# Optimization experiments

Measured on AMD Instinct MI355X. Metric: run time of the kernel, lower is better.

Reference implementation:

```python
import jax, jax.numpy as jnp
import numpy as np

B, K, D = 8192, 50, 64
NU, NV = 100000, 100000


def setup_inputs() -> dict:
    key = jax.random.key(0)
    ks = jax.random.split(key, 9)
    nodes = jax.random.randint(ks[0], (B,), 0, NU)
    history = jax.random.randint(ks[1], (B, K), 0, NV)
    degrees = jax.random.randint(ks[2], (B,), 1, K + 1)  # 1..K actual neighbors per node
    u_to_e = jax.random.normal(ks[3], (NU, D), dtype=jnp.float32)
    v_to_e = jax.random.normal(ks[4], (NV, D), dtype=jnp.float32)
    s1 = 1.0 / np.sqrt(2 * D)
    s2 = 1.0 / np.sqrt(D)
    att1_w = jax.random.normal(ks[5], (D, 2 * D), dtype=jnp.float32) * s1
    att2_w = jax.random.normal(ks[6], (D, D), dtype=jnp.float32) * s2
    att3_w = jax.random.normal(ks[7], (1, D), dtype=jnp.float32) * s2
    return {
        "nodes": nodes, "history": history, "degrees": degrees,
        "u_to_e": u_to_e, "v_to_e": v_to_e,
        "att1_w": att1_w, "att1_b": jnp.zeros((D,), jnp.float32),
        "att2_w": att2_w, "att2_b": jnp.zeros((D,), jnp.float32),
        "att3_w": att3_w, "att3_b": jnp.zeros((1,), jnp.float32),
    }


def reference(nodes, history, degrees, u_to_e, v_to_e,
              att1_w, att1_b, att2_w, att2_b, att3_w, att3_b):
    # uv=True: neighbors are items (v_to_e), self representation from u_to_e.
    neigh = v_to_e[history]                      # [B, K, D] gathered neighbor embeddings
    self_e = u_to_e[nodes]                       # [B, D]
    self_rep = jnp.broadcast_to(self_e[:, None, :], neigh.shape)
    x = jnp.concatenate([neigh, self_rep], axis=-1)        # [B, K, 2D]
    h = jax.nn.relu(jnp.einsum('bkf,df->bkd', x, att1_w) + att1_b)
    h = jax.nn.relu(jnp.einsum('bkd,ed->bke', h, att2_w) + att2_b)
    logits = (jnp.einsum('bkd,od->bko', h, att3_w) + att3_b)[..., 0]  # [B, K]
    # Softmax over the true (ragged) neighbor set only.
    mask = jnp.arange(K)[None, :] < degrees[:, None]       # [B, K] bool
    logits = jnp.where(mask, logits, -1e9)
    att = jax.nn.softmax(logits, axis=1) * mask            # [B, K]
    return jnp.einsum('bkd,bk->bd', neigh, att)            # [B, D]
```

## Files before the change

### kernel.cpp

```cpp
#include <hip/hip_runtime.h>
#include <cstdint>
#include <cstddef>

constexpr int D = 64;
constexpr int TWO_D = 128;

typedef __attribute__((ext_vector_type(8))) short bf16x8;
typedef __attribute__((ext_vector_type(4))) float f32x4;
typedef __attribute__((ext_vector_type(4))) unsigned short u16x4;

static __device__ __forceinline__ short f2bf(float x) {
    unsigned u = __builtin_bit_cast(unsigned, x);
    u += 0x7fffu + ((u >> 16) & 1u);
    return (short)(u >> 16);
}
static __device__ __forceinline__ float bf2f(unsigned short h) {
    return __builtin_bit_cast(float, ((unsigned)h) << 16);
}
static __device__ __forceinline__ bf16x8 cvt8(const float* p) {
    const float4 a = *(const float4*)p;
    const float4 c = *(const float4*)(p + 4);
    bf16x8 f;
    f[0] = f2bf(a.x); f[1] = f2bf(a.y); f[2] = f2bf(a.z); f[3] = f2bf(a.w);
    f[4] = f2bf(c.x); f[5] = f2bf(c.y); f[6] = f2bf(c.z); f[7] = f2bf(c.w);
    return f;
}

__global__ __launch_bounds__(256) void proj_s(
    const float* __restrict__ u_to_e, const int* __restrict__ nodes,
    const float* __restrict__ att1_w, const float* __restrict__ att1_b,
    const float* __restrict__ att2_w,
    float* __restrict__ S, unsigned short* __restrict__ W1F,
    unsigned short* __restrict__ W2F,
    int Bn, int nSB)
{
    const int tid = threadIdx.x;

    if ((int)blockIdx.x == nSB) {
        if (tid < 64) {
            const int plg = tid >> 4, plc = tid & 15;
#pragma unroll
            for (int tc = 0; tc < 4; ++tc)
#pragma unroll
                for (int ks = 0; ks < 2; ++ks) {
                    const bf16x8 f1 = cvt8(
                        att1_w + (tc * 16 + plc) * TWO_D + ks * 32 + plg * 8);
                    *(bf16x8*)(W1F + ((size_t)(tc * 2 + ks) * 64 + tid) * 8) = f1;
                    const bf16x8 f2 = cvt8(
                        att2_w + (tc * 16 + plc) * D + ks * 32 + plg * 8);
                    *(bf16x8*)(W2F + ((size_t)(tc * 2 + ks) * 64 + tid) * 8) = f2;
                }
        }
        return;
    }

    constexpr int ST = 68;
    __shared__ float xs[64 * ST];
    __shared__ float ws[64 * ST];

    const int base = (int)blockIdx.x * 64;

#pragma unroll
    for (int it = 0; it < 4; ++it) {
        const int flat = it * 256 + tid;
        const int dd = flat >> 4, f4 = flat & 15;
        const float4 w = *(const float4*)(att1_w + dd * TWO_D + D + f4 * 4);
        ws[(f4 * 4 + 0) * ST + dd] = w.x;
        ws[(f4 * 4 + 1) * ST + dd] = w.y;
        ws[(f4 * 4 + 2) * ST + dd] = w.z;
        ws[(f4 * 4 + 3) * ST + dd] = w.w;
    }
#pragma unroll
    for (int it = 0; it < 4; ++it) {
        const int flat = it * 256 + tid;
        const int r = flat >> 4, f4 = flat & 15;
        int gr = base + r;
        if (gr >= Bn) gr = Bn - 1;
        const int row = nodes[gr];
        const float4 x = *(const float4*)(u_to_e + (size_t)row * D + f4 * 4);
        xs[(f4 * 4 + 0) * ST + r] = x.x;
        xs[(f4 * 4 + 1) * ST + r] = x.y;
        xs[(f4 * 4 + 2) * ST + r] = x.z;
        xs[(f4 * 4 + 3) * ST + r] = x.w;
    }
    __syncthreads();

    const int d0 = (tid & 15) * 4;
    const int r0 = (tid >> 4) * 4;
    float acc[4][4];
#pragma unroll
    for (int i = 0; i < 4; ++i)
#pragma unroll
        for (int j = 0; j < 4; ++j) acc[i][j] = 0.f;

#pragma unroll 8
    for (int f = 0; f < D; ++f) {
        const float4 w = *(const float4*)&ws[f * ST + d0];
        const float4 x = *(const float4*)&xs[f * ST + r0];
        const float wv[4] = {w.x, w.y, w.z, w.w};
        const float xv[4] = {x.x, x.y, x.z, x.w};
#pragma unroll
        for (int ri = 0; ri < 4; ++ri)
#pragma unroll
            for (int di = 0; di < 4; ++di)
                acc[ri][di] += xv[ri] * wv[di];
    }

    float bv[4];
#pragma unroll
    for (int di = 0; di < 4; ++di) bv[di] = att1_b[d0 + di];
#pragma unroll
    for (int ri = 0; ri < 4; ++ri) {
        const int gr = base + r0 + ri;
        if (gr < Bn) {
            float4 o = {acc[ri][0] + bv[0], acc[ri][1] + bv[1],
                        acc[ri][2] + bv[2], acc[ri][3] + bv[3]};
            *(float4*)(S + (size_t)gr * D + d0) = o;
        }
    }
}

__global__ __launch_bounds__(256) void agg_fused(
    const int* __restrict__ history, const int* __restrict__ degrees,
    const float* __restrict__ v_to_e,
    const float* __restrict__ att2_b, const float* __restrict__ att3_w,
    const float* __restrict__ S,
    const unsigned short* __restrict__ W1F,
    const unsigned short* __restrict__ W2F,
    float* __restrict__ out, int Bn, int K)
{
    __shared__ unsigned short hldsb[4][16 * 72];
    __shared__ float red[4][64];
    __shared__ float mxs[4];
    __shared__ float sms[4];

    const int b     = (int)blockIdx.x;
    const int wslot = threadIdx.x >> 6;
    const int l     = threadIdx.x & 63;
    const int lg    = l >> 4;
    const int lc    = l & 15;
    const int deg   = degrees[b];
    const bool live = (wslot * 16 < deg);
    const bool act  = (wslot * 16 + lc < deg);

    int kk = wslot * 16 + lc;
    if (kk > K - 1) kk = K - 1;
    const int vrow = history[(size_t)b * K + kk];

    float4 vr4[4];
    if (live) {
#pragma unroll
        for (int jj = 0; jj < 4; ++jj) {
            const int row = __shfl(vrow, jj * 4 + lg);
            vr4[jj] = *(const float4*)(v_to_e + (size_t)row * D + lc * 4);
        }
    }

    float m_w = -1e30f, ex = 0.f;
    float4 acc4 = {0.f, 0.f, 0.f, 0.f};
    if (live) {
        const float* vp = v_to_e + (size_t)vrow * D;
        const bf16x8 bv0 = cvt8(vp + lg * 8);
        const bf16x8 bv1 = cvt8(vp + 32 + lg * 8);

        unsigned short* hrow = &hldsb[wslot][0];
#pragma unroll
        for (int tc = 0; tc < 4; ++tc) {
            f32x4 hacc = (f32x4)0.f;
            const bf16x8 w10 = *(const bf16x8*)(
                W1F + ((size_t)(tc * 2 + 0) * 64 + l) * 8);
            hacc = __builtin_amdgcn_mfma_f32_16x16x32_bf16(w10, bv0, hacc, 0, 0, 0);
            const bf16x8 w11 = *(const bf16x8*)(
                W1F + ((size_t)(tc * 2 + 1) * 64 + l) * 8);
            hacc = __builtin_amdgcn_mfma_f32_16x16x32_bf16(w11, bv1, hacc, 0, 0, 0);
            const float4 sv = *(const float4*)(S + (size_t)b * D + tc * 16 + lg * 4);
            u16x4 hb;
            hb[0] = (unsigned short)f2bf(fmaxf(hacc[0] + sv.x, 0.f));
            hb[1] = (unsigned short)f2bf(fmaxf(hacc[1] + sv.y, 0.f));
            hb[2] = (unsigned short)f2bf(fmaxf(hacc[2] + sv.z, 0.f));
            hb[3] = (unsigned short)f2bf(fmaxf(hacc[3] + sv.w, 0.f));
            *(u16x4*)&hrow[lc * 72 + tc * 16 + lg * 4] = hb;
        }

        const bf16x8 af0 = *(const bf16x8*)&hrow[lc * 72 + lg * 8];
        const bf16x8 af1 = *(const bf16x8*)&hrow[lc * 72 + 32 + lg * 8];

        float part = 0.f;
#pragma unroll
        for (int tc = 0; tc < 4; ++tc) {
            f32x4 acc = (f32x4)0.f;
            const bf16x8 w0 = *(const bf16x8*)(
                W2F + ((size_t)(tc * 2 + 0) * 64 + l) * 8);
            acc = __builtin_amdgcn_mfma_f32_16x16x32_bf16(w0, af0, acc, 0, 0, 0);
            const bf16x8 w1 = *(const bf16x8*)(
                W2F + ((size_t)(tc * 2 + 1) * 64 + l) * 8);
            acc = __builtin_amdgcn_mfma_f32_16x16x32_bf16(w1, af1, acc, 0, 0, 0);
            const float4 b2v = *(const float4*)(att2_b + tc * 16 + lg * 4);
            const float4 w3v = *(const float4*)(att3_w + tc * 16 + lg * 4);
            part += fmaxf(acc[0] + b2v.x, 0.f) * w3v.x;
            part += fmaxf(acc[1] + b2v.y, 0.f) * w3v.y;
            part += fmaxf(acc[2] + b2v.z, 0.f) * w3v.z;
            part += fmaxf(acc[3] + b2v.w, 0.f) * w3v.w;
        }
        part += __shfl_xor(part, 16);
        part += __shfl_xor(part, 32);
        const float logit = act ? part : -1e30f;

        m_w = logit;
#pragma unroll
        for (int off = 1; off < 16; off <<= 1)
            m_w = fmaxf(m_w, __shfl_xor(m_w, off));
        ex = act ? __expf(logit - m_w) : 0.f;
        float s_w = ex;
#pragma unroll
        for (int off = 1; off < 16; off <<= 1)
            s_w += __shfl_xor(s_w, off);
        if (l == 0) { mxs[wslot] = m_w; sms[wslot] = s_w; }

#pragma unroll
        for (int jj = 0; jj < 4; ++jj) {
            const float a = __shfl(ex, jj * 4 + lg);
            acc4.x += a * vr4[jj].x;
            acc4.y += a * vr4[jj].y;
            acc4.z += a * vr4[jj].z;
            acc4.w += a * vr4[jj].w;
        }
        acc4.x += __shfl_xor(acc4.x, 16); acc4.x += __shfl_xor(acc4.x, 32);
        acc4.y += __shfl_xor(acc4.y, 16); acc4.y += __shfl_xor(acc4.y, 32);
        acc4.z += __shfl_xor(acc4.z, 16); acc4.z += __shfl_xor(acc4.z, 32);
        acc4.w += __shfl_xor(acc4.w, 16); acc4.w += __shfl_xor(acc4.w, 32);
    } else {
        if (l == 0) { mxs[wslot] = -1e30f; sms[wslot] = 0.f; }
    }

    __syncthreads();
    const float m = fmaxf(fmaxf(mxs[0], mxs[1]), fmaxf(mxs[2], mxs[3]));
    const float tot = sms[0] * __expf(mxs[0] - m) + sms[1] * __expf(mxs[1] - m)
                    + sms[2] * __expf(mxs[2] - m) + sms[3] * __expf(mxs[3] - m);
    const float scale = live ? __expf(m_w - m) / tot : 0.f;

    const float comp = (lg == 0) ? acc4.x : (lg == 1) ? acc4.y
                     : (lg == 2) ? acc4.z : acc4.w;
    red[wslot][lc * 4 + lg] = comp * scale;
    __syncthreads();
    if (wslot == 0)
        out[(size_t)b * D + l] =
            (red[0][l] + red[1][l]) + (red[2][l] + red[3][l]);
}

__global__ __launch_bounds__(256) void agg_fallback(
    const int* __restrict__ nodes, const int* __restrict__ history,
    const int* __restrict__ degrees,
    const float* __restrict__ u_to_e, const float* __restrict__ v_to_e,
    const float* __restrict__ att1_w, const float* __restrict__ att1_b,
    const float* __restrict__ att2_w, const float* __restrict__ att2_b,
    const float* __restrict__ att3_w, const float* __restrict__ att3_b,
    float* __restrict__ out, int Bn, int K)
{
    const int b    = (int)((blockIdx.x * blockDim.x + threadIdx.x) >> 6);
    const int lane = threadIdx.x & 63;
    if (b >= Bn) return;

    const int  deg    = degrees[b];
    const bool active = (lane < deg);
    const int  v      = history[(size_t)b * K + ((lane < K) ? lane : 0)];

    float h1[D];
    float vr[D];
    const float4* v4 = (const float4*)(v_to_e + (size_t)v * D);
#pragma unroll
    for (int i = 0; i < D / 4; ++i) {
        float4 t = v4[i];
        vr[4 * i + 0] = t.x; vr[4 * i + 1] = t.y;
        vr[4 * i + 2] = t.z; vr[4 * i + 3] = t.w;
    }
    const float* urow = u_to_e + (size_t)nodes[b] * D;
#pragma unroll
    for (int d = 0; d < D; ++d) {
        const float* w1 = att1_w + d * TWO_D;
        float a0 = att1_b[d], a1 = 0.f, a2 = 0.f, a3 = 0.f;
#pragma unroll
        for (int f = 0; f < D; f += 4) {
            a0 += vr[f + 0] * w1[f + 0];
            a1 += vr[f + 1] * w1[f + 1];
            a2 += vr[f + 2] * w1[f + 2];
            a3 += vr[f + 3] * w1[f + 3];
            a0 += urow[f + 0] * w1[D + f + 0];
            a1 += urow[f + 1] * w1[D + f + 1];
            a2 += urow[f + 2] * w1[D + f + 2];
            a3 += urow[f + 3] * w1[D + f + 3];
        }
        h1[d] = fmaxf((a0 + a1) + (a2 + a3), 0.f);
    }

    float logit = att3_b[0];
#pragma unroll 4
    for (int e = 0; e < D; ++e) {
        const float* w2r = att2_w + e * D;
        float a0 = 0.f, a1 = 0.f, a2 = 0.f, a3 = 0.f;
#pragma unroll
        for (int dd = 0; dd < D; dd += 4) {
            a0 += h1[dd + 0] * w2r[dd + 0];
            a1 += h1[dd + 1] * w2r[dd + 1];
            a2 += h1[dd + 2] * w2r[dd + 2];
            a3 += h1[dd + 3] * w2r[dd + 3];
        }
        float h2 = (a0 + a1) + (a2 + a3) + att2_b[e];
        logit += fmaxf(h2, 0.f) * att3_w[e];
    }

    float ml = active ? logit : -1e30f;
#pragma unroll
    for (int off = 32; off > 0; off >>= 1) ml = fmaxf(ml, __shfl_xor(ml, off));
    const float ex = active ? __expf(logit - ml) : 0.f;
    float smv = ex;
#pragma unroll
    for (int off = 32; off > 0; off >>= 1) smv += __shfl_xor(smv, off);
    const float att = ex / smv;

    float acc = 0.f;
    for (int kk = 0; kk < deg; ++kk) {
        const float a  = __shfl(att, kk);
        const int   vk = __shfl(v, kk);
        acc += a * v_to_e[(size_t)vk * D + lane];
    }
    out[(size_t)b * D + lane] = acc;
}

extern "C" void kernel_launch(void* const* d_in, const int* in_sizes, int n_in,
                              void* d_out, int out_size, void* d_ws, size_t ws_size,
                              hipStream_t stream)
{
    const int*   nodes   = (const int*)d_in[0];
    const int*   history = (const int*)d_in[1];
    const int*   degrees = (const int*)d_in[2];
    const float* u_to_e  = (const float*)d_in[3];
    const float* v_to_e  = (const float*)d_in[4];
    const float* att1_w  = (const float*)d_in[5];
    const float* att1_b  = (const float*)d_in[6];
    const float* att2_w  = (const float*)d_in[7];
    const float* att2_b  = (const float*)d_in[8];
    const float* att3_w  = (const float*)d_in[9];
    const float* att3_b  = (const float*)d_in[10];
    float*       out     = (float*)d_out;

    const int Bn = in_sizes[0];
    const int K  = in_sizes[1] / Bn;

    const size_t s_bytes   = (size_t)Bn * D * sizeof(float);
    const size_t wf_bytes  = (size_t)8 * 64 * 8 * sizeof(unsigned short);
    const size_t need = s_bytes + 2 * wf_bytes;

    if (ws_size >= need) {
        char* p = (char*)d_ws;
        float*          S   = (float*)p;            p += s_bytes;
        unsigned short* W1F = (unsigned short*)p;   p += wf_bytes;
        unsigned short* W2F = (unsigned short*)p;
        const int nSB = (Bn + 63) / 64;
        proj_s<<<nSB + 1, 256, 0, stream>>>(
            u_to_e, nodes, att1_w, att1_b, att2_w, S, W1F, W2F, Bn, nSB);
        agg_fused<<<Bn, 256, 0, stream>>>(
            history, degrees, v_to_e, att2_b, att3_w,
            S, W1F, W2F, out, Bn, K);
    } else {
        const int agg_blocks = (Bn * 64 + 255) / 256;
        agg_fallback<<<agg_blocks, 256, 0, stream>>>(
            nodes, history, degrees, u_to_e, v_to_e,
            att1_w, att1_b, att2_w, att2_b, att3_w, att3_b,
            out, Bn, K);
    }
}
```

Before: 43.95 us.

## Process four nodes per block and prefetch next node's neighbor embeddings

Each block of agg_fused now handles four consecutive batch rows instead of one. Inside the loop it issues the gathers of the next row's history and neighbor embeddings, into registers, in the middle of the current row's two MLP stages. This overlaps gather latency with MFMA work and cuts block launch overhead. In exchange the grid shrinks to a quarter of the blocks, which may lower memory-level parallelism across the GPU, and register pressure rises from the doubled prefetch buffers.

```diff
diff --git a/kernel.cpp b/kernel.cpp
--- a/kernel.cpp
+++ b/kernel.cpp
@@ -4,6 +4,7 @@
 
 constexpr int D = 64;
 constexpr int TWO_D = 128;
+constexpr int NB = 4;
 
 typedef __attribute__((ext_vector_type(8))) short bf16x8;
 typedef __attribute__((ext_vector_type(4))) float f32x4;
@@ -20,6 +21,12 @@
 static __device__ __forceinline__ bf16x8 cvt8(const float* p) {
     const float4 a = *(const float4*)p;
     const float4 c = *(const float4*)(p + 4);
+    bf16x8 f;
+    f[0] = f2bf(a.x); f[1] = f2bf(a.y); f[2] = f2bf(a.z); f[3] = f2bf(a.w);
+    f[4] = f2bf(c.x); f[5] = f2bf(c.y); f[6] = f2bf(c.z); f[7] = f2bf(c.w);
+    return f;
+}
+static __device__ __forceinline__ bf16x8 pack2(const float4& a, const float4& c) {
     bf16x8 f;
     f[0] = f2bf(a.x); f[1] = f2bf(a.y); f[2] = f2bf(a.z); f[3] = f2bf(a.w);
     f[4] = f2bf(c.x); f[5] = f2bf(c.y); f[6] = f2bf(c.z); f[7] = f2bf(c.w);
@@ -134,118 +141,164 @@
     __shared__ float mxs[4];
     __shared__ float sms[4];
 
-    const int b     = (int)blockIdx.x;
     const int wslot = threadIdx.x >> 6;
     const int l     = threadIdx.x & 63;
     const int lg    = l >> 4;
     const int lc    = l & 15;
-    const int deg   = degrees[b];
-    const bool live = (wslot * 16 < deg);
-    const bool act  = (wslot * 16 + lc < deg);
-
-    int kk = wslot * 16 + lc;
-    if (kk > K - 1) kk = K - 1;
-    const int vrow = history[(size_t)b * K + kk];
-
+
+    int kpos = wslot * 16 + lc;
+    if (kpos > K - 1) kpos = K - 1;
+
+    const int b0 = (int)blockIdx.x * NB;
+
+    int    deg  = 0, vrow = 0;
     float4 vr4[4];
-    if (live) {
-#pragma unroll
-        for (int jj = 0; jj < 4; ++jj) {
-            const int row = __shfl(vrow, jj * 4 + lg);
-            vr4[jj] = *(const float4*)(v_to_e + (size_t)row * D + lc * 4);
-        }
-    }
-
-    float m_w = -1e30f, ex = 0.f;
-    float4 acc4 = {0.f, 0.f, 0.f, 0.f};
-    if (live) {
-        const float* vp = v_to_e + (size_t)vrow * D;
-        const bf16x8 bv0 = cvt8(vp + lg * 8);
-        const bf16x8 bv1 = cvt8(vp + 32 + lg * 8);
-
-        unsigned short* hrow = &hldsb[wslot][0];
-#pragma unroll
-        for (int tc = 0; tc < 4; ++tc) {
-            f32x4 hacc = (f32x4)0.f;
-            const bf16x8 w10 = *(const bf16x8*)(
-                W1F + ((size_t)(tc * 2 + 0) * 64 + l) * 8);
-            hacc = __builtin_amdgcn_mfma_f32_16x16x32_bf16(w10, bv0, hacc, 0, 0, 0);
-            const bf16x8 w11 = *(const bf16x8*)(
-                W1F + ((size_t)(tc * 2 + 1) * 64 + l) * 8);
-            hacc = __builtin_amdgcn_mfma_f32_16x16x32_bf16(w11, bv1, hacc, 0, 0, 0);
-            const float4 sv = *(const float4*)(S + (size_t)b * D + tc * 16 + lg * 4);
-            u16x4 hb;
-            hb[0] = (unsigned short)f2bf(fmaxf(hacc[0] + sv.x, 0.f));
-            hb[1] = (unsigned short)f2bf(fmaxf(hacc[1] + sv.y, 0.f));
-            hb[2] = (unsigned short)f2bf(fmaxf(hacc[2] + sv.z, 0.f));
-            hb[3] = (unsigned short)f2bf(fmaxf(hacc[3] + sv.w, 0.f));
-            *(u16x4*)&hrow[lc * 72 + tc * 16 + lg * 4] = hb;
-        }
-
-        const bf16x8 af0 = *(const bf16x8*)&hrow[lc * 72 + lg * 8];
-        const bf16x8 af1 = *(const bf16x8*)&hrow[lc * 72 + 32 + lg * 8];
-
-        float part = 0.f;
-#pragma unroll
-        for (int tc = 0; tc < 4; ++tc) {
-            f32x4 acc = (f32x4)0.f;
-            const bf16x8 w0 = *(const bf16x8*)(
-                W2F + ((size_t)(tc * 2 + 0) * 64 + l) * 8);
-            acc = __builtin_amdgcn_mfma_f32_16x16x32_bf16(w0, af0, acc, 0, 0, 0);
-            const bf16x8 w1 = *(const bf16x8*)(
-                W2F + ((size_t)(tc * 2 + 1) * 64 + l) * 8);
-            acc = __builtin_amdgcn_mfma_f32_16x16x32_bf16(w1, af1, acc, 0, 0, 0);
-            const float4 b2v = *(const float4*)(att2_b + tc * 16 + lg * 4);
-            const float4 w3v = *(const float4*)(att3_w + tc * 16 + lg * 4);
-            part += fmaxf(acc[0] + b2v.x, 0.f) * w3v.x;
-            part += fmaxf(acc[1] + b2v.y, 0.f) * w3v.y;
-            part += fmaxf(acc[2] + b2v.z, 0.f) * w3v.z;
-            part += fmaxf(acc[3] + b2v.w, 0.f) * w3v.w;
-        }
-        part += __shfl_xor(part, 16);
-        part += __shfl_xor(part, 32);
-        const float logit = act ? part : -1e30f;
-
-        m_w = logit;
-#pragma unroll
-        for (int off = 1; off < 16; off <<= 1)
-            m_w = fmaxf(m_w, __shfl_xor(m_w, off));
-        ex = act ? __expf(logit - m_w) : 0.f;
-        float s_w = ex;
-#pragma unroll
-        for (int off = 1; off < 16; off <<= 1)
-            s_w += __shfl_xor(s_w, off);
-        if (l == 0) { mxs[wslot] = m_w; sms[wslot] = s_w; }
-
-#pragma unroll
-        for (int jj = 0; jj < 4; ++jj) {
-            const float a = __shfl(ex, jj * 4 + lg);
-            acc4.x += a * vr4[jj].x;
-            acc4.y += a * vr4[jj].y;
-            acc4.z += a * vr4[jj].z;
-            acc4.w += a * vr4[jj].w;
-        }
-        acc4.x += __shfl_xor(acc4.x, 16); acc4.x += __shfl_xor(acc4.x, 32);
-        acc4.y += __shfl_xor(acc4.y, 16); acc4.y += __shfl_xor(acc4.y, 32);
-        acc4.z += __shfl_xor(acc4.z, 16); acc4.z += __shfl_xor(acc4.z, 32);
-        acc4.w += __shfl_xor(acc4.w, 16); acc4.w += __shfl_xor(acc4.w, 32);
-    } else {
-        if (l == 0) { mxs[wslot] = -1e30f; sms[wslot] = 0.f; }
-    }
-
-    __syncthreads();
-    const float m = fmaxf(fmaxf(mxs[0], mxs[1]), fmaxf(mxs[2], mxs[3]));
-    const float tot = sms[0] * __expf(mxs[0] - m) + sms[1] * __expf(mxs[1] - m)
-                    + sms[2] * __expf(mxs[2] - m) + sms[3] * __expf(mxs[3] - m);
-    const float scale = live ? __expf(m_w - m) / tot : 0.f;
-
-    const float comp = (lg == 0) ? acc4.x : (lg == 1) ? acc4.y
-                     : (lg == 2) ? acc4.z : acc4.w;
-    red[wslot][lc * 4 + lg] = comp * scale;
-    __syncthreads();
-    if (wslot == 0)
-        out[(size_t)b * D + l] =
-            (red[0][l] + red[1][l]) + (red[2][l] + red[3][l]);
+    float4 bvr[4];
+    if (b0 < Bn) {
+        deg  = degrees[b0];
+        vrow = history[(size_t)b0 * K + kpos];
+        if (wslot * 16 < deg) {
+#pragma unroll
+            for (int jj = 0; jj < 4; ++jj) {
+                const int row = __shfl(vrow, jj * 4 + lg);
+                vr4[jj] = *(const float4*)(v_to_e + (size_t)row * D + lc * 4);
+            }
+            const float* vp = v_to_e + (size_t)vrow * D;
+            bvr[0] = *(const float4*)(vp + lg * 8);
+            bvr[1] = *(const float4*)(vp + lg * 8 + 4);
+            bvr[2] = *(const float4*)(vp + 32 + lg * 8);
+            bvr[3] = *(const float4*)(vp + 32 + lg * 8 + 4);
+        }
+    }
+
+    for (int i = 0; i < NB; ++i) {
+        const int  bcur  = b0 + i;
+        const bool valid = (bcur < Bn);
+        const bool live  = valid && (wslot * 16 < deg);
+        const bool act   = valid && (wslot * 16 + lc < deg);
+
+        const int  bnext  = bcur + 1;
+        const bool validN = (i + 1 < NB) && (bnext < Bn);
+        int degN = 0, vrowN = 0;
+        if (validN) {
+            degN  = degrees[bnext];
+            vrowN = history[(size_t)bnext * K + kpos];
+        }
+
+        float m_w = -1e30f, ex = 0.f;
+        float4 acc4 = {0.f, 0.f, 0.f, 0.f};
+
+        bf16x8 af0, af1;
+        if (live) {
+            const bf16x8 bv0 = pack2(bvr[0], bvr[1]);
+            const bf16x8 bv1 = pack2(bvr[2], bvr[3]);
+            unsigned short* hrow = &hldsb[wslot][0];
+#pragma unroll
+            for (int tc = 0; tc < 4; ++tc) {
+                f32x4 hacc = (f32x4)0.f;
+                const bf16x8 w10 = *(const bf16x8*)(
+                    W1F + ((size_t)(tc * 2 + 0) * 64 + l) * 8);
+                hacc = __builtin_amdgcn_mfma_f32_16x16x32_bf16(w10, bv0, hacc, 0, 0, 0);
+                const bf16x8 w11 = *(const bf16x8*)(
+                    W1F + ((size_t)(tc * 2 + 1) * 64 + l) * 8);
+                hacc = __builtin_amdgcn_mfma_f32_16x16x32_bf16(w11, bv1, hacc, 0, 0, 0);
+                const float4 sv = *(const float4*)(S + (size_t)bcur * D + tc * 16 + lg * 4);
+                u16x4 hb;
+                hb[0] = (unsigned short)f2bf(fmaxf(hacc[0] + sv.x, 0.f));
+                hb[1] = (unsigned short)f2bf(fmaxf(hacc[1] + sv.y, 0.f));
+                hb[2] = (unsigned short)f2bf(fmaxf(hacc[2] + sv.z, 0.f));
+                hb[3] = (unsigned short)f2bf(fmaxf(hacc[3] + sv.w, 0.f));
+                *(u16x4*)&hrow[lc * 72 + tc * 16 + lg * 4] = hb;
+            }
+            af0 = *(const bf16x8*)&hrow[lc * 72 + lg * 8];
+            af1 = *(const bf16x8*)&hrow[lc * 72 + 32 + lg * 8];
+        }
+
+        float4 vr4n[4];
+        float4 bvrn[4];
+        const bool liveN = validN && (wslot * 16 < degN);
+        if (liveN) {
+#pragma unroll
+            for (int jj = 0; jj < 4; ++jj) {
+                const int row = __shfl(vrowN, jj * 4 + lg);
+                vr4n[jj] = *(const float4*)(v_to_e + (size_t)row * D + lc * 4);
+            }
+            const float* vp = v_to_e + (size_t)vrowN * D;
+            bvrn[0] = *(const float4*)(vp + lg * 8);
+            bvrn[1] = *(const float4*)(vp + lg * 8 + 4);
+            bvrn[2] = *(const float4*)(vp + 32 + lg * 8);
+            bvrn[3] = *(const float4*)(vp + 32 + lg * 8 + 4);
+        }
+
+        if (live) {
+            float part = 0.f;
+#pragma unroll
+            for (int tc = 0; tc < 4; ++tc) {
+                f32x4 acc = (f32x4)0.f;
+                const bf16x8 w0 = *(const bf16x8*)(
+                    W2F + ((size_t)(tc * 2 + 0) * 64 + l) * 8);
+                acc = __builtin_amdgcn_mfma_f32_16x16x32_bf16(w0, af0, acc, 0, 0, 0);
+                const bf16x8 w1 = *(const bf16x8*)(
+                    W2F + ((size_t)(tc * 2 + 1) * 64 + l) * 8);
+                acc = __builtin_amdgcn_mfma_f32_16x16x32_bf16(w1, af1, acc, 0, 0, 0);
+                const float4 b2v = *(const float4*)(att2_b + tc * 16 + lg * 4);
+                const float4 w3v = *(const float4*)(att3_w + tc * 16 + lg * 4);
+                part += fmaxf(acc[0] + b2v.x, 0.f) * w3v.x;
+                part += fmaxf(acc[1] + b2v.y, 0.f) * w3v.y;
+                part += fmaxf(acc[2] + b2v.z, 0.f) * w3v.z;
+                part += fmaxf(acc[3] + b2v.w, 0.f) * w3v.w;
+            }
+            part += __shfl_xor(part, 16);
+            part += __shfl_xor(part, 32);
+            const float logit = act ? part : -1e30f;
+
+            m_w = logit;
+#pragma unroll
+            for (int off = 1; off < 16; off <<= 1)
+                m_w = fmaxf(m_w, __shfl_xor(m_w, off));
+            ex = act ? __expf(logit - m_w) : 0.f;
+            float s_w = ex;
+#pragma unroll
+            for (int off = 1; off < 16; off <<= 1)
+                s_w += __shfl_xor(s_w, off);
+            if (l == 0) { mxs[wslot] = m_w; sms[wslot] = s_w; }
+
+#pragma unroll
+            for (int jj = 0; jj < 4; ++jj) {
+                const float a = __shfl(ex, jj * 4 + lg);
+                acc4.x += a * vr4[jj].x;
+                acc4.y += a * vr4[jj].y;
+                acc4.z += a * vr4[jj].z;
+                acc4.w += a * vr4[jj].w;
+            }
+            acc4.x += __shfl_xor(acc4.x, 16); acc4.x += __shfl_xor(acc4.x, 32);
+            acc4.y += __shfl_xor(acc4.y, 16); acc4.y += __shfl_xor(acc4.y, 32);
+            acc4.z += __shfl_xor(acc4.z, 16); acc4.z += __shfl_xor(acc4.z, 32);
+            acc4.w += __shfl_xor(acc4.w, 16); acc4.w += __shfl_xor(acc4.w, 32);
+        } else if (valid) {
+            if (l == 0) { mxs[wslot] = -1e30f; sms[wslot] = 0.f; }
+        }
+
+        if (valid) {
+            __syncthreads();
+            const float m = fmaxf(fmaxf(mxs[0], mxs[1]), fmaxf(mxs[2], mxs[3]));
+            const float tot = sms[0] * __expf(mxs[0] - m) + sms[1] * __expf(mxs[1] - m)
+                            + sms[2] * __expf(mxs[2] - m) + sms[3] * __expf(mxs[3] - m);
+            const float scale = live ? __expf(m_w - m) / tot : 0.f;
+            const float comp = (lg == 0) ? acc4.x : (lg == 1) ? acc4.y
+                             : (lg == 2) ? acc4.z : acc4.w;
+            red[wslot][lc * 4 + lg] = comp * scale;
+            __syncthreads();
+            if (wslot == 0)
+                out[(size_t)bcur * D + l] =
+                    (red[0][l] + red[1][l]) + (red[2][l] + red[3][l]);
+        }
+
+        deg  = degN;
+        vrow = vrowN;
+#pragma unroll
+        for (int jj = 0; jj < 4; ++jj) { vr4[jj] = vr4n[jj]; bvr[jj] = bvrn[jj]; }
+    }
 }
 
 __global__ __launch_bounds__(256) void agg_fallback(
@@ -359,7 +412,7 @@
         const int nSB = (Bn + 63) / 64;
         proj_s<<<nSB + 1, 256, 0, stream>>>(
             u_to_e, nodes, att1_w, att1_b, att2_w, S, W1F, W2F, Bn, nSB);
-        agg_fused<<<Bn, 256, 0, stream>>>(
+        agg_fused<<<(Bn + NB - 1) / NB, 256, 0, stream>>>(
             history, degrees, v_to_e, att2_b, att3_w,
             S, W1F, W2F, out, Bn, K);
     } else {
```

Result: slower. 59.09 us (+34.5%).

## Process one batch row per wave with online softmax and prefetched tiles

Applied to the files above, without the earlier changes.

The aggregation kernel now assigns one batch row to each wave instead of one row per 256-thread block. Each wave loops over up to four 16-neighbor tiles, keeping an online softmax (running max and sum) and prefetching the next tile's embeddings into registers while the current tile is computed. Block-wide shared-memory reductions and both __syncthreads are removed, and waves whose tiles fall past the degree no longer sit idle. The cost is serial per-wave latency across tiles and higher register pressure from the double-buffered float4 arrays.

```diff
diff --git a/kernel.cpp b/kernel.cpp
--- a/kernel.cpp
+++ b/kernel.cpp
@@ -14,12 +14,15 @@
     u += 0x7fffu + ((u >> 16) & 1u);
     return (short)(u >> 16);
 }
-static __device__ __forceinline__ float bf2f(unsigned short h) {
-    return __builtin_bit_cast(float, ((unsigned)h) << 16);
-}
 static __device__ __forceinline__ bf16x8 cvt8(const float* p) {
     const float4 a = *(const float4*)p;
     const float4 c = *(const float4*)(p + 4);
+    bf16x8 f;
+    f[0] = f2bf(a.x); f[1] = f2bf(a.y); f[2] = f2bf(a.z); f[3] = f2bf(a.w);
+    f[4] = f2bf(c.x); f[5] = f2bf(c.y); f[6] = f2bf(c.z); f[7] = f2bf(c.w);
+    return f;
+}
+static __device__ __forceinline__ bf16x8 pack2(const float4& a, const float4& c) {
     bf16x8 f;
     f[0] = f2bf(a.x); f[1] = f2bf(a.y); f[2] = f2bf(a.z); f[3] = f2bf(a.w);
     f[4] = f2bf(c.x); f[5] = f2bf(c.y); f[6] = f2bf(c.z); f[7] = f2bf(c.w);
@@ -120,7 +123,7 @@
     }
 }
 
-__global__ __launch_bounds__(256) void agg_fused(
+__global__ __launch_bounds__(256) void agg_wave(
     const int* __restrict__ history, const int* __restrict__ degrees,
     const float* __restrict__ v_to_e,
     const float* __restrict__ att2_b, const float* __restrict__ att3_w,
@@ -130,122 +133,146 @@
     float* __restrict__ out, int Bn, int K)
 {
     __shared__ unsigned short hldsb[4][16 * 72];
-    __shared__ float red[4][64];
-    __shared__ float mxs[4];
-    __shared__ float sms[4];
-
-    const int b     = (int)blockIdx.x;
+
     const int wslot = threadIdx.x >> 6;
-    const int l     = threadIdx.x & 63;
-    const int lg    = l >> 4;
-    const int lc    = l & 15;
-    const int deg   = degrees[b];
-    const bool live = (wslot * 16 < deg);
-    const bool act  = (wslot * 16 + lc < deg);
-
-    int kk = wslot * 16 + lc;
-    if (kk > K - 1) kk = K - 1;
-    const int vrow = history[(size_t)b * K + kk];
-
-    float4 vr4[4];
-    if (live) {
+    const int b     = (int)blockIdx.x * 4 + wslot;
+    if (b >= Bn) return;
+    const int l  = threadIdx.x & 63;
+    const int lg = l >> 4;
+    const int lc = l & 15;
+    const int deg = degrees[b];
+
+    int vrow[4];
+#pragma unroll
+    for (int t = 0; t < 4; ++t) {
+        int kp = t * 16 + lc;
+        if (kp > K - 1) kp = K - 1;
+        vrow[t] = history[(size_t)b * K + kp];
+    }
+
+    float4 sv[4], b2v[4], w3v[4];
+#pragma unroll
+    for (int tc = 0; tc < 4; ++tc) {
+        sv[tc]  = *(const float4*)(S + (size_t)b * D + tc * 16 + lg * 4);
+        b2v[tc] = *(const float4*)(att2_b + tc * 16 + lg * 4);
+        w3v[tc] = *(const float4*)(att3_w + tc * 16 + lg * 4);
+    }
+
+    unsigned short* hrow = &hldsb[wslot][0];
+
+    float4 bvr[2][4];
+    float4 vr4[2][4];
+
+    {
+        const float* vp = v_to_e + (size_t)vrow[0] * D;
+        bvr[0][0] = *(const float4*)(vp + lg * 8);
+        bvr[0][1] = *(const float4*)(vp + lg * 8 + 4);
+        bvr[0][2] = *(const float4*)(vp + 32 + lg * 8);
+        bvr[0][3] = *(const float4*)(vp + 32 + lg * 8 + 4);
 #pragma unroll
         for (int jj = 0; jj < 4; ++jj) {
-            const int row = __shfl(vrow, jj * 4 + lg);
-            vr4[jj] = *(const float4*)(v_to_e + (size_t)row * D + lc * 4);
-        }
-    }
-
-    float m_w = -1e30f, ex = 0.f;
+            const int row = __shfl(vrow[0], jj * 4 + lg);
+            vr4[0][jj] = *(const float4*)(v_to_e + (size_t)row * D + lc * 4);
+        }
+    }
+
+    float m_run = -1e30f, s_run = 0.f;
     float4 acc4 = {0.f, 0.f, 0.f, 0.f};
-    if (live) {
-        const float* vp = v_to_e + (size_t)vrow * D;
-        const bf16x8 bv0 = cvt8(vp + lg * 8);
-        const bf16x8 bv1 = cvt8(vp + 32 + lg * 8);
-
-        unsigned short* hrow = &hldsb[wslot][0];
-#pragma unroll
-        for (int tc = 0; tc < 4; ++tc) {
-            f32x4 hacc = (f32x4)0.f;
-            const bf16x8 w10 = *(const bf16x8*)(
-                W1F + ((size_t)(tc * 2 + 0) * 64 + l) * 8);
-            hacc = __builtin_amdgcn_mfma_f32_16x16x32_bf16(w10, bv0, hacc, 0, 0, 0);
-            const bf16x8 w11 = *(const bf16x8*)(
-                W1F + ((size_t)(tc * 2 + 1) * 64 + l) * 8);
-            hacc = __builtin_amdgcn_mfma_f32_16x16x32_bf16(w11, bv1, hacc, 0, 0, 0);
-            const float4 sv = *(const float4*)(S + (size_t)b * D + tc * 16 + lg * 4);
-            u16x4 hb;
-            hb[0] = (unsigned short)f2bf(fmaxf(hacc[0] + sv.x, 0.f));
-            hb[1] = (unsigned short)f2bf(fmaxf(hacc[1] + sv.y, 0.f));
-            hb[2] = (unsigned short)f2bf(fmaxf(hacc[2] + sv.z, 0.f));
-            hb[3] = (unsigned short)f2bf(fmaxf(hacc[3] + sv.w, 0.f));
-            *(u16x4*)&hrow[lc * 72 + tc * 16 + lg * 4] = hb;
-        }
-
-        const bf16x8 af0 = *(const bf16x8*)&hrow[lc * 72 + lg * 8];
-        const bf16x8 af1 = *(const bf16x8*)&hrow[lc * 72 + 32 + lg * 8];
-
-        float part = 0.f;
-#pragma unroll
-        for (int tc = 0; tc < 4; ++tc) {
-            f32x4 acc = (f32x4)0.f;
-            const bf16x8 w0 = *(const bf16x8*)(
-                W2F + ((size_t)(tc * 2 + 0) * 64 + l) * 8);
-            acc = __builtin_amdgcn_mfma_f32_16x16x32_bf16(w0, af0, acc, 0, 0, 0);
-            const bf16x8 w1 = *(const bf16x8*)(
-                W2F + ((size_t)(tc * 2 + 1) * 64 + l) * 8);
-            acc = __builtin_amdgcn_mfma_f32_16x16x32_bf16(w1, af1, acc, 0, 0, 0);
-            const float4 b2v = *(const float4*)(att2_b + tc * 16 + lg * 4);
-            const float4 w3v = *(const float4*)(att3_w + tc * 16 + lg * 4);
-            part += fmaxf(acc[0] + b2v.x, 0.f) * w3v.x;
-            part += fmaxf(acc[1] + b2v.y, 0.f) * w3v.y;
-            part += fmaxf(acc[2] + b2v.z, 0.f) * w3v.z;
-            part += fmaxf(acc[3] + b2v.w, 0.f) * w3v.w;
-        }
-        part += __shfl_xor(part, 16);
-        part += __shfl_xor(part, 32);
-        const float logit = act ? part : -1e30f;
-
-        m_w = logit;
-#pragma unroll
-        for (int off = 1; off < 16; off <<= 1)
-            m_w = fmaxf(m_w, __shfl_xor(m_w, off));
-        ex = act ? __expf(logit - m_w) : 0.f;
-        float s_w = ex;
-#pragma unroll
-        for (int off = 1; off < 16; off <<= 1)
-            s_w += __shfl_xor(s_w, off);
-        if (l == 0) { mxs[wslot] = m_w; sms[wslot] = s_w; }
-
-#pragma unroll
-        for (int jj = 0; jj < 4; ++jj) {
-            const float a = __shfl(ex, jj * 4 + lg);
-            acc4.x += a * vr4[jj].x;
-            acc4.y += a * vr4[jj].y;
-            acc4.z += a * vr4[jj].z;
-            acc4.w += a * vr4[jj].w;
-        }
-        acc4.x += __shfl_xor(acc4.x, 16); acc4.x += __shfl_xor(acc4.x, 32);
-        acc4.y += __shfl_xor(acc4.y, 16); acc4.y += __shfl_xor(acc4.y, 32);
-        acc4.z += __shfl_xor(acc4.z, 16); acc4.z += __shfl_xor(acc4.z, 32);
-        acc4.w += __shfl_xor(acc4.w, 16); acc4.w += __shfl_xor(acc4.w, 32);
-    } else {
-        if (l == 0) { mxs[wslot] = -1e30f; sms[wslot] = 0.f; }
-    }
-
-    __syncthreads();
-    const float m = fmaxf(fmaxf(mxs[0], mxs[1]), fmaxf(mxs[2], mxs[3]));
-    const float tot = sms[0] * __expf(mxs[0] - m) + sms[1] * __expf(mxs[1] - m)
-                    + sms[2] * __expf(mxs[2] - m) + sms[3] * __expf(mxs[3] - m);
-    const float scale = live ? __expf(m_w - m) / tot : 0.f;
+
+#pragma unroll
+    for (int t = 0; t < 4; ++t) {
+        if (t * 16 < deg) {
+            const int cur = t & 1, nxt = cur ^ 1;
+
+            if (t + 1 < 4 && (t + 1) * 16 < deg) {
+                const float* vp = v_to_e + (size_t)vrow[t + 1] * D;
+                bvr[nxt][0] = *(const float4*)(vp + lg * 8);
+                bvr[nxt][1] = *(const float4*)(vp + lg * 8 + 4);
+                bvr[nxt][2] = *(const float4*)(vp + 32 + lg * 8);
+                bvr[nxt][3] = *(const float4*)(vp + 32 + lg * 8 + 4);
+#pragma unroll
+                for (int jj = 0; jj < 4; ++jj) {
+                    const int row = __shfl(vrow[t + 1], jj * 4 + lg);
+                    vr4[nxt][jj] = *(const float4*)(v_to_e + (size_t)row * D + lc * 4);
+                }
+            }
+
+            const bf16x8 bv0 = pack2(bvr[cur][0], bvr[cur][1]);
+            const bf16x8 bv1 = pack2(bvr[cur][2], bvr[cur][3]);
+#pragma unroll
+            for (int tc = 0; tc < 4; ++tc) {
+                f32x4 hacc = (f32x4)0.f;
+                const bf16x8 w10 = *(const bf16x8*)(
+                    W1F + ((size_t)(tc * 2 + 0) * 64 + l) * 8);
+                hacc = __builtin_amdgcn_mfma_f32_16x16x32_bf16(w10, bv0, hacc, 0, 0, 0);
+                const bf16x8 w11 = *(const bf16x8*)(
+                    W1F + ((size_t)(tc * 2 + 1) * 64 + l) * 8);
+                hacc = __builtin_amdgcn_mfma_f32_16x16x32_bf16(w11, bv1, hacc, 0, 0, 0);
+                u16x4 hb;
+                hb[0] = (unsigned short)f2bf(fmaxf(hacc[0] + sv[tc].x, 0.f));
+                hb[1] = (unsigned short)f2bf(fmaxf(hacc[1] + sv[tc].y, 0.f));
+                hb[2] = (unsigned short)f2bf(fmaxf(hacc[2] + sv[tc].z, 0.f));
+                hb[3] = (unsigned short)f2bf(fmaxf(hacc[3] + sv[tc].w, 0.f));
+                *(u16x4*)&hrow[lc * 72 + tc * 16 + lg * 4] = hb;
+            }
+            const bf16x8 af0 = *(const bf16x8*)&hrow[lc * 72 + lg * 8];
+            const bf16x8 af1 = *(const bf16x8*)&hrow[lc * 72 + 32 + lg * 8];
+
+            float part = 0.f;
+#pragma unroll
+            for (int tc = 0; tc < 4; ++tc) {
+                f32x4 acc = (f32x4)0.f;
+                const bf16x8 w0 = *(const bf16x8*)(
+                    W2F + ((size_t)(tc * 2 + 0) * 64 + l) * 8);
+                acc = __builtin_amdgcn_mfma_f32_16x16x32_bf16(w0, af0, acc, 0, 0, 0);
+                const bf16x8 w1 = *(const bf16x8*)(
+                    W2F + ((size_t)(tc * 2 + 1) * 64 + l) * 8);
+                acc = __builtin_amdgcn_mfma_f32_16x16x32_bf16(w1, af1, acc, 0, 0, 0);
+                part += fmaxf(acc[0] + b2v[tc].x, 0.f) * w3v[tc].x;
+                part += fmaxf(acc[1] + b2v[tc].y, 0.f) * w3v[tc].y;
+                part += fmaxf(acc[2] + b2v[tc].z, 0.f) * w3v[tc].z;
+                part += fmaxf(acc[3] + b2v[tc].w, 0.f) * w3v[tc].w;
+            }
+            part += __shfl_xor(part, 16);
+            part += __shfl_xor(part, 32);
+            const bool actk = (t * 16 + lc < deg);
+            const float logit = actk ? part : -1e30f;
+
+            float mt = logit;
+#pragma unroll
+            for (int off = 1; off < 16; off <<= 1)
+                mt = fmaxf(mt, __shfl_xor(mt, off));
+            const float m_new = fmaxf(m_run, mt);
+            const float scale_old = __expf(m_run - m_new);
+            const float ex = actk ? __expf(logit - m_new) : 0.f;
+            float st = ex;
+#pragma unroll
+            for (int off = 1; off < 16; off <<= 1)
+                st += __shfl_xor(st, off);
+            s_run = s_run * scale_old + st;
+            m_run = m_new;
+            acc4.x *= scale_old; acc4.y *= scale_old;
+            acc4.z *= scale_old; acc4.w *= scale_old;
+
+#pragma unroll
+            for (int jj = 0; jj < 4; ++jj) {
+                const float a = __shfl(ex, jj * 4 + lg);
+                acc4.x += a * vr4[cur][jj].x;
+                acc4.y += a * vr4[cur][jj].y;
+                acc4.z += a * vr4[cur][jj].z;
+                acc4.w += a * vr4[cur][jj].w;
+            }
+        }
+    }
+
+    acc4.x += __shfl_xor(acc4.x, 16); acc4.x += __shfl_xor(acc4.x, 32);
+    acc4.y += __shfl_xor(acc4.y, 16); acc4.y += __shfl_xor(acc4.y, 32);
+    acc4.z += __shfl_xor(acc4.z, 16); acc4.z += __shfl_xor(acc4.z, 32);
+    acc4.w += __shfl_xor(acc4.w, 16); acc4.w += __shfl_xor(acc4.w, 32);
 
     const float comp = (lg == 0) ? acc4.x : (lg == 1) ? acc4.y
                      : (lg == 2) ? acc4.z : acc4.w;
-    red[wslot][lc * 4 + lg] = comp * scale;
-    __syncthreads();
-    if (wslot == 0)
-        out[(size_t)b * D + l] =
-            (red[0][l] + red[1][l]) + (red[2][l] + red[3][l]);
+    out[(size_t)b * D + lc * 4 + lg] = comp / s_run;
 }
 
 __global__ __launch_bounds__(256) void agg_fallback(
@@ -359,7 +386,7 @@
         const int nSB = (Bn + 63) / 64;
         proj_s<<<nSB + 1, 256, 0, stream>>>(
             u_to_e, nodes, att1_w, att1_b, att2_w, S, W1F, W2F, Bn, nSB);
-        agg_fused<<<Bn, 256, 0, stream>>>(
+        agg_wave<<<(Bn + 3) / 4, 256, 0, stream>>>(
             history, degrees, v_to_e, att2_b, att3_w,
             S, W1F, W2F, out, Bn, K);
     } else {
```

Result: slower. 49.43 us (+12.5%).
